# Optimization experiments

Hardware: AMD Instinct MI355X
Metric: run time of the kernel (lower is better)

## Reference

```python
import jax, jax.numpy as jnp
import numpy as np

HIDDEN = 4096
INTER = 11008
B, S = 8, 16
QMAX = 127  # int8 symmetric range for w_bits=8


def setup_inputs() -> dict:
    key = jax.random.key(0)
    ks = jax.random.split(key, 7)
    hidden_state = jax.random.normal(ks[0], (B, S, HIDDEN), dtype=jnp.float32)
    # Quantized weights stored as integer values in float32 (as the dequant source)
    w1_q = jax.random.randint(ks[1], (INTER, HIDDEN), -QMAX - 1, QMAX + 1).astype(jnp.float32)
    w3_q = jax.random.randint(ks[2], (INTER, HIDDEN), -QMAX - 1, QMAX + 1).astype(jnp.float32)
    w2_q = jax.random.randint(ks[3], (HIDDEN, INTER), -QMAX - 1, QMAX + 1).astype(jnp.float32)
    # Per-output-channel dequant scales (has_scale=True)
    w1_s = jax.random.uniform(ks[4], (INTER,), dtype=jnp.float32, minval=0.5, maxval=1.5) * 0.01
    w3_s = jax.random.uniform(ks[5], (INTER,), dtype=jnp.float32, minval=0.5, maxval=1.5) * 0.01
    w2_s = jax.random.uniform(ks[6], (HIDDEN,), dtype=jnp.float32, minval=0.5, maxval=1.5) * 0.01
    return {"hidden_state": hidden_state, "w1_q": w1_q, "w1_s": w1_s,
            "w3_q": w3_q, "w3_s": w3_s, "w2_q": w2_q, "w2_s": w2_s}


def _dequant_linear(x, w_q, w_s):
    # w_q: [out, in] integer-valued weights; w_s: [out] per-channel scale
    # y = x @ (w_q * w_s[:, None]).T == (x @ w_q.T) * w_s
    return jnp.einsum('bsh,oh->bso', x, w_q) * w_s


def reference(hidden_state, w1_q, w1_s, w3_q, w3_s, w2_q, w2_s):
    up = _dequant_linear(hidden_state, w1_q, w1_s)      # [B,S,INTER]
    gate = _dequant_linear(hidden_state, w3_q, w3_s)    # [B,S,INTER]
    h = jax.nn.silu(up) * gate                          # SwiGLU
    return _dequant_linear(h, w2_q, w2_s)               # [B,S,HIDDEN]
```

## Files before the change

### kernel.cpp

```cpp
#include <hip/hip_runtime.h>

#define HIDDEN 4096
#define INTER  11008
#define MTOK   128
#define NMERG  (2*INTER)
#define KS1    4
#define KS2    16

typedef short          short8  __attribute__((ext_vector_type(8)));
typedef unsigned short ushort8 __attribute__((ext_vector_type(8)));
typedef float          f32x16  __attribute__((ext_vector_type(16)));
#define AS1 __attribute__((address_space(1)))
#define AS3 __attribute__((address_space(3)))

static __device__ __forceinline__ unsigned short f2bf_rne(float f) {
    unsigned u = __builtin_bit_cast(unsigned, f);
    u += 0x7FFFu + ((u >> 16) & 1u);
    return (unsigned short)(u >> 16);
}
static __device__ __forceinline__ float bf2f(unsigned short b) {
    unsigned u = (unsigned)b << 16;
    return __builtin_bit_cast(float, u);
}
static __device__ __forceinline__ int pk2(float lo, float hi) {
    return (int)__builtin_amdgcn_perm(__builtin_bit_cast(unsigned, hi),
                                      __builtin_bit_cast(unsigned, lo),
                                      0x07060302u);
}

__global__ void cvt_x_k(const float* __restrict__ x, unsigned short* __restrict__ A2) {
    int f = blockIdx.x * 256 + threadIdx.x;
    int lane = f & 63, w = f >> 6;
    int kstep = w >> 2, ms = w & 3;
    int m = ms * 32 + (lane & 31);
    int k = kstep * 16 + (lane >> 5) * 8;
    const float* src = x + (size_t)m * HIDDEN + k;
    float4 v0 = *(const float4*)(src);
    float4 v1 = *(const float4*)(src + 4);
    ushort8 o;
    o[0] = f2bf_rne(v0.x); o[1] = f2bf_rne(v0.y); o[2] = f2bf_rne(v0.z); o[3] = f2bf_rne(v0.w);
    o[4] = f2bf_rne(v1.x); o[5] = f2bf_rne(v1.y); o[6] = f2bf_rne(v1.z); o[7] = f2bf_rne(v1.w);
    *(ushort8*)(A2 + (size_t)f * 8) = o;
}

template<bool OBF16>
__global__ __launch_bounds__(256) void gemm_k(
    const unsigned short* __restrict__ A2,
    const float* __restrict__ B0, const float* __restrict__ B1, int nhalf,
    void* __restrict__ part, int K, int N, int totTiles, int ksplit)
{
    __shared__ __align__(16) float lds[8192];
    const int lane = threadIdx.x & 63;
    const int ws   = threadIdx.x >> 6;
    const int n0   = blockIdx.x * 128;
    const int ks   = blockIdx.y;
    const int tbeg = (ks * totTiles) / ksplit;
    const int tend = ((ks + 1) * totTiles) / ksplit;

    const char* gbase[8];
#pragma unroll
    for (int i = 0; i < 8; ++i) {
        int s = ws * 512 + i * 64 + lane;
        int n = s >> 4;
        int a = (s & 15) ^ (n & 15);
        const float* rowp = (n0 + n < nhalf) ? (B0 + (size_t)(n0 + n) * K)
                                             : (B1 + (size_t)(n0 + n - nhalf) * K);
        gbase[i] = (const char*)rowp + a * 16;
    }

    f32x16 acc[4];
#pragma unroll
    for (int t = 0; t < 4; ++t)
#pragma unroll
        for (int r = 0; r < 16; ++r) acc[t][r] = 0.f;

    const int nl = ws * 32 + (lane & 31);

    for (int t = tbeg; t < tend; ++t) {
        const size_t koff = (size_t)t * 64 * 4;
#pragma unroll
        for (int i = 0; i < 8; ++i) {
            __builtin_amdgcn_global_load_lds(
                (const AS1 unsigned*)(gbase[i] + koff),
                (AS3 unsigned*)((char*)lds + ws * 8192 + i * 1024), 16, 0, 0);
        }
        __syncthreads();

#pragma unroll
        for (int step = 0; step < 4; ++step) {
            int a0 = step * 4 + ((lane >> 5) << 1);
            int p0 = nl * 16 + (a0 ^ (nl & 15));
            int p1 = nl * 16 + ((a0 + 1) ^ (nl & 15));
            float4 v0 = *(const float4*)((const char*)lds + p0 * 16);
            float4 v1 = *(const float4*)((const char*)lds + p1 * 16);
            int4 bi;
            bi.x = pk2(v0.x, v0.y); bi.y = pk2(v0.z, v0.w);
            bi.z = pk2(v1.x, v1.y); bi.w = pk2(v1.z, v1.w);
            short8 bf = __builtin_bit_cast(short8, bi);
            int kg = t * 4 + step;
#pragma unroll
            for (int ms = 0; ms < 4; ++ms) {
                short8 af = *(const short8*)(A2 + ((size_t)(kg * 4 + ms) * 64 + lane) * 8);
                acc[ms] = __builtin_amdgcn_mfma_f32_32x32x16_bf16(af, bf, acc[ms], 0, 0, 0);
            }
        }
        __syncthreads();
    }

    const int n = n0 + ws * 32 + (lane & 31);
#pragma unroll
    for (int ms = 0; ms < 4; ++ms)
#pragma unroll
        for (int r = 0; r < 16; ++r) {
            int m = ms * 32 + (r & 3) + 8 * (r >> 2) + 4 * (lane >> 5);
            size_t idx = ((size_t)ks * MTOK + m) * (size_t)N + n;
            if (OBF16) ((unsigned short*)part)[idx] = f2bf_rne(acc[ms][r]);
            else       ((float*)part)[idx] = acc[ms][r];
        }
}

__global__ void swiglu_k(const unsigned short* __restrict__ p1,
                         const float* __restrict__ s1, const float* __restrict__ s3,
                         unsigned short* __restrict__ h2)
{
    int f = blockIdx.x * 256 + threadIdx.x;
    int lane = f & 63, w = f >> 6;
    int kstep = w >> 2, ms = w & 3;
    int m = ms * 32 + (lane & 31);
    int j = kstep * 16 + (lane >> 5) * 8;
    float up[8], gt[8];
#pragma unroll
    for (int e = 0; e < 8; ++e) { up[e] = 0.f; gt[e] = 0.f; }
#pragma unroll
    for (int ks = 0; ks < KS1; ++ks) {
        const unsigned short* pu = p1 + ((size_t)ks * MTOK + m) * NMERG + j;
        ushort8 u = *(const ushort8*)(pu);
        ushort8 g = *(const ushort8*)(pu + INTER);
#pragma unroll
        for (int e = 0; e < 8; ++e) { up[e] += bf2f(u[e]); gt[e] += bf2f(g[e]); }
    }
    float4 c1a = *(const float4*)(s1 + j), c1b = *(const float4*)(s1 + j + 4);
    float4 c3a = *(const float4*)(s3 + j), c3b = *(const float4*)(s3 + j + 4);
    float c1[8] = {c1a.x, c1a.y, c1a.z, c1a.w, c1b.x, c1b.y, c1b.z, c1b.w};
    float c3[8] = {c3a.x, c3a.y, c3a.z, c3a.w, c3b.x, c3b.y, c3b.z, c3b.w};
    ushort8 o;
#pragma unroll
    for (int e = 0; e < 8; ++e) {
        float u = up[e] * c1[e], g = gt[e] * c3[e];
        o[e] = f2bf_rne(g * u / (1.f + __expf(-u)));
    }
    *(ushort8*)(h2 + (size_t)f * 8) = o;
}

__global__ void reduce_k(const float* __restrict__ p, const float* __restrict__ s2,
                         float* __restrict__ out)
{
    int i = (blockIdx.x * 256 + threadIdx.x) * 4;
    float4 acc = *(const float4*)(p + i);
#pragma unroll
    for (int s = 1; s < KS2; ++s) {
        float4 v = *(const float4*)(p + (size_t)s * MTOK * HIDDEN + i);
        acc.x += v.x; acc.y += v.y; acc.z += v.z; acc.w += v.w;
    }
    int ncol = i & (HIDDEN - 1);
    float4 sc = *(const float4*)(s2 + ncol);
    acc.x *= sc.x; acc.y *= sc.y; acc.z *= sc.z; acc.w *= sc.w;
    *(float4*)(out + i) = acc;
}

extern "C" void kernel_launch(void* const* d_in, const int* in_sizes, int n_in,
                              void* d_out, int out_size, void* d_ws, size_t ws_size,
                              hipStream_t stream) {
    const float* x   = (const float*)d_in[0];
    const float* w1q = (const float*)d_in[1];
    const float* w1s = (const float*)d_in[2];
    const float* w3q = (const float*)d_in[3];
    const float* w3s = (const float*)d_in[4];
    const float* w2q = (const float*)d_in[5];
    const float* w2s = (const float*)d_in[6];
    float* out = (float*)d_out;

    char* ws = (char*)d_ws;
    unsigned short* xb2 = (unsigned short*)ws;
    unsigned short* h2  = (unsigned short*)(ws + (1u << 20));
    void* part          = (void*)(ws + (4u << 20));

    cvt_x_k<<<MTOK * HIDDEN / 8 / 256, 256, 0, stream>>>(x, xb2);
    gemm_k<true><<<dim3(NMERG / 128, KS1), 256, 0, stream>>>(
        xb2, w1q, w3q, INTER, part, HIDDEN, NMERG, HIDDEN / 64, KS1);
    swiglu_k<<<MTOK * INTER / 8 / 256, 256, 0, stream>>>(
        (const unsigned short*)part, w1s, w3s, h2);
    gemm_k<false><<<dim3(HIDDEN / 128, KS2), 256, 0, stream>>>(
        h2, w2q, w2q, 1 << 30, part, INTER, HIDDEN, INTER / 64, KS2);
    reduce_k<<<MTOK * HIDDEN / 4 / 256, 256, 0, stream>>>(
        (const float*)part, w2s, out);
}
```

Before: 539.0 us.

## Replace LDS-staged weight tiles with direct register double-buffered loads per wave

The GEMM kernel no longer stages fp32 weight tiles through LDS with global_load_lds and two barriers per tile. Each wave now reads its own 32 weight rows straight from global memory into registers and software-pipelines two k-steps ahead, removing all block-level synchronisation. It also adds an occupancy hint to the launch bounds. The cost is more register pressure and less coalesced 32-byte-per-lane global reads, with no data sharing between waves.

Result: slower. 576.1 us (+6.9%).

```diff
diff --git a/kernel.cpp b/kernel.cpp
--- a/kernel.cpp
+++ b/kernel.cpp
@@ -10,8 +10,6 @@
 typedef short          short8  __attribute__((ext_vector_type(8)));
 typedef unsigned short ushort8 __attribute__((ext_vector_type(8)));
 typedef float          f32x16  __attribute__((ext_vector_type(16)));
-#define AS1 __attribute__((address_space(1)))
-#define AS3 __attribute__((address_space(3)))
 
 static __device__ __forceinline__ unsigned short f2bf_rne(float f) {
     unsigned u = __builtin_bit_cast(unsigned, f);
@@ -44,29 +42,24 @@
 }
 
 template<bool OBF16>
-__global__ __launch_bounds__(256) void gemm_k(
+__global__ __launch_bounds__(256, 3) void gemm_k(
     const unsigned short* __restrict__ A2,
     const float* __restrict__ B0, const float* __restrict__ B1, int nhalf,
-    void* __restrict__ part, int K, int N, int totTiles, int ksplit)
+    void* __restrict__ part, int K, int N, int stepsTot, int ksplit)
 {
-    __shared__ __align__(16) float lds[8192];
     const int lane = threadIdx.x & 63;
     const int ws   = threadIdx.x >> 6;
-    const int n0   = blockIdx.x * 128;
+    const int wq   = blockIdx.x * 4 + ws;
+    const int n0   = wq * 32;
     const int ks   = blockIdx.y;
-    const int tbeg = (ks * totTiles) / ksplit;
-    const int tend = ((ks + 1) * totTiles) / ksplit;
+    const int sbeg = (ks * stepsTot) / ksplit;
+    const int send = ((ks + 1) * stepsTot) / ksplit;
 
-    const char* gbase[8];
-#pragma unroll
-    for (int i = 0; i < 8; ++i) {
-        int s = ws * 512 + i * 64 + lane;
-        int n = s >> 4;
-        int a = (s & 15) ^ (n & 15);
-        const float* rowp = (n0 + n < nhalf) ? (B0 + (size_t)(n0 + n) * K)
-                                             : (B1 + (size_t)(n0 + n - nhalf) * K);
-        gbase[i] = (const char*)rowp + a * 16;
-    }
+    const int n = n0 + (lane & 31);
+    const float* rp = (n < nhalf) ? B0 + (size_t)n * K
+                                  : B1 + (size_t)(n - nhalf) * K;
+    const char* rb = (const char*)rp + (lane >> 5) * 32;
+    const unsigned short* ab = A2 + (size_t)lane * 8;
 
     f32x16 acc[4];
 #pragma unroll
@@ -74,46 +67,46 @@
 #pragma unroll
         for (int r = 0; r < 16; ++r) acc[t][r] = 0.f;
 
-    const int nl = ws * 32 + (lane & 31);
+    float4 b0[2], b1[2];
+    short8 a0[4], a1[4];
 
-    for (int t = tbeg; t < tend; ++t) {
-        const size_t koff = (size_t)t * 64 * 4;
+    auto loadB = [&](int s, float4 (&b)[2]) {
+        b[0] = *(const float4*)(rb + (size_t)s * 64);
+        b[1] = *(const float4*)(rb + (size_t)s * 64 + 16);
+    };
+    auto loadA = [&](int s, short8 (&a)[4]) {
 #pragma unroll
-        for (int i = 0; i < 8; ++i) {
-            __builtin_amdgcn_global_load_lds(
-                (const AS1 unsigned*)(gbase[i] + koff),
-                (AS3 unsigned*)((char*)lds + ws * 8192 + i * 1024), 16, 0, 0);
+        for (int ms = 0; ms < 4; ++ms)
+            a[ms] = *(const short8*)(ab + (size_t)(s * 4 + ms) * 64 * 8);
+    };
+    auto comp = [&](float4 (&b)[2], short8 (&a)[4]) {
+        int4 bi;
+        bi.x = pk2(b[0].x, b[0].y); bi.y = pk2(b[0].z, b[0].w);
+        bi.z = pk2(b[1].x, b[1].y); bi.w = pk2(b[1].z, b[1].w);
+        short8 bf = __builtin_bit_cast(short8, bi);
+#pragma unroll
+        for (int ms = 0; ms < 4; ++ms)
+            acc[ms] = __builtin_amdgcn_mfma_f32_32x32x16_bf16(a[ms], bf, acc[ms], 0, 0, 0);
+    };
+
+    loadB(sbeg, b0); loadA(sbeg, a0);
+    if (send - sbeg > 1) { loadB(sbeg + 1, b1); loadA(sbeg + 1, a1); }
+
+    for (int s = sbeg; s < send; s += 2) {
+        comp(b0, a0);
+        if (s + 2 < send) { loadB(s + 2, b0); loadA(s + 2, a0); }
+        if (s + 1 < send) {
+            comp(b1, a1);
+            if (s + 3 < send) { loadB(s + 3, b1); loadA(s + 3, a1); }
         }
-        __syncthreads();
-
-#pragma unroll
-        for (int step = 0; step < 4; ++step) {
-            int a0 = step * 4 + ((lane >> 5) << 1);
-            int p0 = nl * 16 + (a0 ^ (nl & 15));
-            int p1 = nl * 16 + ((a0 + 1) ^ (nl & 15));
-            float4 v0 = *(const float4*)((const char*)lds + p0 * 16);
-            float4 v1 = *(const float4*)((const char*)lds + p1 * 16);
-            int4 bi;
-            bi.x = pk2(v0.x, v0.y); bi.y = pk2(v0.z, v0.w);
-            bi.z = pk2(v1.x, v1.y); bi.w = pk2(v1.z, v1.w);
-            short8 bf = __builtin_bit_cast(short8, bi);
-            int kg = t * 4 + step;
-#pragma unroll
-            for (int ms = 0; ms < 4; ++ms) {
-                short8 af = *(const short8*)(A2 + ((size_t)(kg * 4 + ms) * 64 + lane) * 8);
-                acc[ms] = __builtin_amdgcn_mfma_f32_32x32x16_bf16(af, bf, acc[ms], 0, 0, 0);
-            }
-        }
-        __syncthreads();
     }
 
-    const int n = n0 + ws * 32 + (lane & 31);
 #pragma unroll
     for (int ms = 0; ms < 4; ++ms)
 #pragma unroll
         for (int r = 0; r < 16; ++r) {
             int m = ms * 32 + (r & 3) + 8 * (r >> 2) + 4 * (lane >> 5);
-            size_t idx = ((size_t)ks * MTOK + m) * (size_t)N + n;
+            size_t idx = ((size_t)ks * MTOK + m) * (size_t)N + (n0 + (lane & 31));
             if (OBF16) ((unsigned short*)part)[idx] = f2bf_rne(acc[ms][r]);
             else       ((float*)part)[idx] = acc[ms][r];
         }
@@ -187,11 +180,11 @@
 
     cvt_x_k<<<MTOK * HIDDEN / 8 / 256, 256, 0, stream>>>(x, xb2);
     gemm_k<true><<<dim3(NMERG / 128, KS1), 256, 0, stream>>>(
-        xb2, w1q, w3q, INTER, part, HIDDEN, NMERG, HIDDEN / 64, KS1);
+        xb2, w1q, w3q, INTER, part, HIDDEN, NMERG, HIDDEN / 16, KS1);
     swiglu_k<<<MTOK * INTER / 8 / 256, 256, 0, stream>>>(
         (const unsigned short*)part, w1s, w3s, h2);
     gemm_k<false><<<dim3(HIDDEN / 128, KS2), 256, 0, stream>>>(
-        h2, w2q, w2q, 1 << 30, part, INTER, HIDDEN, INTER / 64, KS2);
+        h2, w2q, w2q, 1 << 30, part, INTER, HIDDEN, INTER / 16, KS2);
     reduce_k<<<MTOK * HIDDEN / 4 / 256, 256, 0, stream>>>(
         (const float*)part, w2s, out);
 }
```
